# Kernel optimization log

Hardware: AMD Instinct MI355X
Metric: run time of the kernel (lower is better)

## Reference

```python
import jax, jax.numpy as jnp
import numpy as np

B, N, F = 128, 4096, 32
E, H, DEPTH, OUT = 16, 7, 3, 2
EH = E * H


def _ln(x, g, b, eps=1e-6):
    m = jnp.mean(x, axis=-1, keepdims=True)
    v = jnp.mean(jnp.square(x - m), axis=-1, keepdims=True)
    return (x - m) / jnp.sqrt(v + eps) * g + b


def setup_inputs() -> dict:
    key = jax.random.key(0)
    ks = jax.random.split(key, 24)
    s = 0.05
    inp = {
        "X": jax.random.normal(ks[0], (B, N, F), jnp.float32),
        "avail": jax.random.randint(ks[1], (B, N), 0, 2, jnp.int32),
        "W_enc1": jax.random.normal(ks[2], (F, E), jnp.float32) * s,
        "b_enc1": jnp.zeros((E,), jnp.float32),
        "W_enc2": jax.random.normal(ks[3], (E, E), jnp.float32) * s,
        "b_enc2": jnp.zeros((E,), jnp.float32),
        "W_enc3": jax.random.normal(ks[4], (E, E), jnp.float32) * s,
        "b_enc3": jnp.zeros((E,), jnp.float32),
        "g_enc": jnp.ones((E,), jnp.float32),
        "be_enc": jnp.zeros((E,), jnp.float32),
        "W_agg": jax.random.normal(ks[5], (DEPTH, E, H), jnp.float32) * s,
        "b_agg": jnp.zeros((DEPTH, H), jnp.float32),
        "W_phi1": jax.random.normal(ks[6], (DEPTH, E, EH), jnp.float32) * s,
        "b_phi1": jnp.zeros((DEPTH, EH), jnp.float32),
        "W_phi2": jax.random.normal(ks[7], (DEPTH, EH, EH), jnp.float32) * s,
        "b_phi2": jnp.zeros((DEPTH, EH), jnp.float32),
        "g_phi": jnp.ones((DEPTH, EH), jnp.float32),
        "be_phi": jnp.zeros((DEPTH, EH), jnp.float32),
        "W_proj": jax.random.normal(ks[8], (E, OUT), jnp.float32) * s,
        "b_proj": jnp.zeros((OUT,), jnp.float32),
    }
    return inp


def reference(X, avail, W_enc1, b_enc1, W_enc2, b_enc2, W_enc3, b_enc3, g_enc, be_enc,
              W_agg, b_agg, W_phi1, b_phi1, W_phi2, b_phi2, g_phi, be_phi, W_proj, b_proj):
    # init encoder: Dense-relu, Dense-relu, Dense, LayerNorm  -> Z: [B, N, E]
    Z = jax.nn.relu(X @ W_enc1 + b_enc1)
    Z = jax.nn.relu(Z @ W_enc2 + b_enc2)
    Z = Z @ W_enc3 + b_enc3
    Z = _ln(Z, g_enc, be_enc)
    X_embd = Z

    af = avail.astype(Z.dtype)                      # [B, N]
    num_avail = jnp.maximum(jnp.sum(af, axis=1), 1.0)  # [B]

    for d in range(DEPTH):
        # block_type='qua': fc(Z^2) -> [B, N, H]
        fcZ = jnp.square(Z) @ W_agg[d] + b_agg[d]
        # masked mean over the set axis -> Zbar: [B, H]
        Zbar = jnp.einsum('bnh,bn->bh', fcZ, af) / num_avail[:, None]
        # NonlinearMap(X_embd): Dense-relu-Dense-LayerNorm -> [B, N, E*H]
        phi = jax.nn.relu(X_embd @ W_phi1[d] + b_phi1[d])
        phi = phi @ W_phi2[d] + b_phi2[d]
        phi = _ln(phi, g_phi[d], be_phi[d])
        phi_rs = phi.reshape(phi.shape[0], phi.shape[1], H, E)  # [B, N, H, E]
        # delta = mean_h(phi_rs * Zbar[:,None,:,None]) -> [B, N, E]
        delta = jnp.einsum('bnhe,bh->bne', phi_rs, Zbar) / H
        Z = Z + delta

    return Z @ W_proj + b_proj  # [B, N, OUT]
```

## Files before the change

### kernel.cpp

```cpp
#include <hip/hip_runtime.h>
#include <hip/hip_bf16.h>

#define Bb 128
#define Nn 4096
#define Ff 32
#define Ee 16
#define Hh 7
#define EH 112
#define NROW (Bb*Nn)
#define PS 136
#define TPB_TILES 16
#define NBLK (NROW/16/TPB_TILES)

typedef __attribute__((ext_vector_type(8))) short  bf16x8;
typedef __attribute__((ext_vector_type(4))) float  f32x4;
typedef __attribute__((ext_vector_type(4))) unsigned int u32x4;
typedef __attribute__((ext_vector_type(2))) unsigned int u32x2;

__device__ inline unsigned pack2(float a, float b) {
    __hip_bfloat162 h = __float22bfloat162_rn(make_float2(a, b));
    return *reinterpret_cast<unsigned*>(&h);
}
union BF8 { unsigned u[4]; bf16x8 v; u32x4 q; };

__global__ __launch_bounds__(256) void enc_kernel(
    const float* __restrict__ X,
    const float* __restrict__ W1, const float* __restrict__ b1,
    const float* __restrict__ W2, const float* __restrict__ b2,
    const float* __restrict__ W3, const float* __restrict__ b3,
    const float* __restrict__ g,  const float* __restrict__ be,
    unsigned short* __restrict__ XeBF, float* __restrict__ Z)
{
    __shared__ float sW1[Ff*Ee], sW2[Ee*Ee], sW3[Ee*Ee];
    __shared__ float sb1[Ee], sb2[Ee], sb3[Ee], sg[Ee], sbe[Ee];
    int tid = threadIdx.x;
    for (int i = tid; i < Ff*Ee; i += 256) sW1[i] = W1[i];
    for (int i = tid; i < Ee*Ee; i += 256) { sW2[i] = W2[i]; sW3[i] = W3[i]; }
    if (tid < Ee) { sb1[tid]=b1[tid]; sb2[tid]=b2[tid]; sb3[tid]=b3[tid];
                    sg[tid]=g[tid];   sbe[tid]=be[tid]; }
    __syncthreads();

    size_t row = (size_t)blockIdx.x * 256u + (unsigned)tid;
    const float4* xr = reinterpret_cast<const float4*>(X + row * Ff);
    float x[Ff];
    #pragma unroll
    for (int i = 0; i < Ff/4; ++i) {
        float4 v = xr[i];
        x[4*i+0]=v.x; x[4*i+1]=v.y; x[4*i+2]=v.z; x[4*i+3]=v.w;
    }
    float h1[Ee];
    #pragma unroll
    for (int e = 0; e < Ee; ++e) h1[e] = sb1[e];
    #pragma unroll 4
    for (int k = 0; k < Ff; ++k) {
        float xk = x[k];
        #pragma unroll
        for (int e = 0; e < Ee; ++e) h1[e] = fmaf(xk, sW1[k*Ee+e], h1[e]);
    }
    #pragma unroll
    for (int e = 0; e < Ee; ++e) h1[e] = fmaxf(h1[e], 0.f);

    float h2[Ee];
    #pragma unroll
    for (int e = 0; e < Ee; ++e) h2[e] = sb2[e];
    #pragma unroll 4
    for (int k = 0; k < Ee; ++k) {
        float hk = h1[k];
        #pragma unroll
        for (int e = 0; e < Ee; ++e) h2[e] = fmaf(hk, sW2[k*Ee+e], h2[e]);
    }
    #pragma unroll
    for (int e = 0; e < Ee; ++e) h2[e] = fmaxf(h2[e], 0.f);

    float z[Ee];
    #pragma unroll
    for (int e = 0; e < Ee; ++e) z[e] = sb3[e];
    #pragma unroll 4
    for (int k = 0; k < Ee; ++k) {
        float hk = h2[k];
        #pragma unroll
        for (int e = 0; e < Ee; ++e) z[e] = fmaf(hk, sW3[k*Ee+e], z[e]);
    }
    float m = 0.f;
    #pragma unroll
    for (int e = 0; e < Ee; ++e) m += z[e];
    m *= (1.f/Ee);
    float v = 0.f;
    #pragma unroll
    for (int e = 0; e < Ee; ++e) { float d = z[e]-m; v += d*d; }
    v *= (1.f/Ee);
    float inv = rsqrtf(v + 1e-6f);
    #pragma unroll
    for (int e = 0; e < Ee; ++e) z[e] = (z[e]-m)*inv*sg[e] + sbe[e];

    float4* zo = reinterpret_cast<float4*>(Z + row*Ee);
    #pragma unroll
    for (int i = 0; i < Ee/4; ++i) {
        float4 o; o.x=z[4*i]; o.y=z[4*i+1]; o.z=z[4*i+2]; o.w=z[4*i+3];
        zo[i] = o;
    }
    unsigned us[8];
    #pragma unroll
    for (int j = 0; j < 8; ++j) us[j] = pack2(z[2*j], z[2*j+1]);
    u32x4 lo = {us[0],us[1],us[2],us[3]};
    u32x4 hi = {us[4],us[5],us[6],us[7]};
    u32x4* xo = reinterpret_cast<u32x4*>(XeBF + row*Ee);
    xo[0] = lo; xo[1] = hi;
}

__global__ __launch_bounds__(256) void wpack(
    const float* __restrict__ W_phi2, const float* __restrict__ W_phi1,
    unsigned short* __restrict__ W2F, unsigned short* __restrict__ W1F)
{
    int idx = blockIdx.x*256 + threadIdx.x;
    if (idx < 3*28*64) {
        int d = idx / (28*64); int r = idx % (28*64);
        int f = r >> 6, l = r & 63;
        int lg = l >> 4, li = l & 15, mt = f >> 2, kt = f & 3;
        const float* W2g = W_phi2 + (size_t)d*EH*EH;
        unsigned v[4];
        #pragma unroll
        for (int jj = 0; jj < 4; ++jj) {
            int k0 = kt*32 + lg*8 + jj*2;
            float a = (k0   < EH) ? W2g[(size_t)k0*EH     + mt*16 + li] : 0.f;
            float c = (k0+1 < EH) ? W2g[(size_t)(k0+1)*EH + mt*16 + li] : 0.f;
            v[jj] = pack2(a, c);
        }
        u32x4 q = {v[0], v[1], v[2], v[3]};
        *reinterpret_cast<u32x4*>(W2F + (size_t)idx*8) = q;
    } else if (idx < 3*28*64 + 3*7*64) {
        int r2 = idx - 3*28*64;
        int d = r2 / (7*64); int r = r2 % (7*64);
        int mt = r >> 6, l = r & 63;
        int g = l >> 4, i = l & 15;
        const float* W1g = W_phi1 + (size_t)d*Ee*EH;
        unsigned v[4];
        #pragma unroll
        for (int jj = 0; jj < 4; ++jj) {
            float a = 0.f, c = 0.f;
            if (g < 2) {
                a = W1g[(size_t)(g*8 + jj*2)  *EH + mt*16 + i];
                c = W1g[(size_t)(g*8 + jj*2+1)*EH + mt*16 + i];
            }
            v[jj] = pack2(a, c);
        }
        u32x4 q = {v[0], v[1], v[2], v[3]};
        *reinterpret_cast<u32x4*>(W1F + (size_t)r2*8) = q;
    }
}

__global__ __launch_bounds__(256) void zbar_part(
    const float* __restrict__ Z, const int* __restrict__ avail,
    const float* __restrict__ Wagg, const float* __restrict__ bagg,
    float* __restrict__ part)
{
    __shared__ float sW[Ee*Hh];
    __shared__ float sb[Hh];
    __shared__ float red[256][8];
    int b = blockIdx.x >> 3, p = blockIdx.x & 7;
    int tid = threadIdx.x;
    if (tid < Ee*Hh) sW[tid] = Wagg[tid];
    if (tid < Hh)    sb[tid] = bagg[tid];
    __syncthreads();

    float acc[Hh]; float cnt = 0.f;
    #pragma unroll
    for (int h = 0; h < Hh; ++h) acc[h] = 0.f;

    #pragma unroll
    for (int it = 0; it < 2; ++it) {
        int n = p*512 + it*256 + tid;
        size_t row = (size_t)b*Nn + n;
        const float4* zr = reinterpret_cast<const float4*>(Z + row*Ee);
        float zs[Ee];
        #pragma unroll
        for (int i = 0; i < Ee/4; ++i) {
            float4 v = zr[i];
            zs[4*i+0]=v.x*v.x; zs[4*i+1]=v.y*v.y; zs[4*i+2]=v.z*v.z; zs[4*i+3]=v.w*v.w;
        }
        float fc[Hh];
        #pragma unroll
        for (int h = 0; h < Hh; ++h) fc[h] = sb[h];
        #pragma unroll 4
        for (int e = 0; e < Ee; ++e) {
            float ze = zs[e];
            #pragma unroll
            for (int h = 0; h < Hh; ++h) fc[h] = fmaf(ze, sW[e*Hh+h], fc[h]);
        }
        float af = (float)avail[(size_t)b*Nn + n];
        #pragma unroll
        for (int h = 0; h < Hh; ++h) acc[h] = fmaf(af, fc[h], acc[h]);
        cnt += af;
    }
    #pragma unroll
    for (int h = 0; h < Hh; ++h) red[tid][h] = acc[h];
    red[tid][7] = cnt;
    __syncthreads();
    for (int s = 128; s > 0; s >>= 1) {
        if (tid < s) {
            #pragma unroll
            for (int i = 0; i < 8; ++i) red[tid][i] += red[tid+s][i];
        }
        __syncthreads();
    }
    if (tid < 8) part[((size_t)b*8 + p)*8 + tid] = red[0][tid];
}

__global__ __launch_bounds__(1024) void zbar_fin(
    const float* __restrict__ part, float* __restrict__ Zbar)
{
    int tid = threadIdx.x;
    int b = tid >> 3, h = tid & 7;
    float s = 0.f;
    #pragma unroll
    for (int p = 0; p < 8; ++p) s += part[((size_t)b*8 + p)*8 + h];
    float cnt = __shfl(s, (tid & 63) | 7);
    if (h < Hh) Zbar[b*Hh + h] = s / fmaxf(cnt, 1.f);
}

template<bool LAST>
__global__ __launch_bounds__(256, 3) void phi_mfma(
    const unsigned short* __restrict__ Xe,
    float* __restrict__ Z,
    const float* __restrict__ Zbar,
    const unsigned short* __restrict__ W1F,
    const unsigned short* __restrict__ W2F,
    const float* __restrict__ b1g, const float* __restrict__ b2g,
    const float* __restrict__ gg,  const float* __restrict__ beg,
    const float* __restrict__ Wp,  const float* __restrict__ bp,
    float* __restrict__ out)
{
    __shared__ __align__(16) unsigned short sW2F[28*512];
    __shared__ __align__(16) unsigned short sP1[4][16*PS];
    __shared__ __align__(16) float sB1[EH], sB2[EH];

    int tid  = threadIdx.x;
    int wave = tid >> 6, lane = tid & 63;
    int g = lane >> 4, i = lane & 15;

    for (int p = tid; p < 28*64; p += 256)
        *reinterpret_cast<u32x4*>(&sW2F[p*8]) =
            *reinterpret_cast<const u32x4*>(W2F + (size_t)p*8);
    for (int p = tid; p < (4*16*PS)/8; p += 256) {
        u32x4 zq = {0u,0u,0u,0u};
        reinterpret_cast<u32x4*>(&sP1[0][0])[p] = zq;
    }
    if (tid < EH) { sB1[tid] = b1g[tid]; sB2[tid] = b2g[tid]; }

    bf16x8 aW1[7];
    #pragma unroll
    for (int mt = 0; mt < 7; ++mt)
        aW1[mt] = *reinterpret_cast<const bf16x8*>(W1F + (size_t)(mt*64 + lane)*8);

    int b = blockIdx.x / (Nn/(TPB_TILES*16));
    f32x4 gz[7];
    float Gz[4] = {0,0,0,0}, Bz[4] = {0,0,0,0};
    #pragma unroll
    for (int mt = 0; mt < 7; ++mt) {
        float zbm = Zbar[b*Hh + mt] * (1.f/Hh);
        f32x4 pg = *reinterpret_cast<const f32x4*>(gg  + mt*16 + 4*g);
        f32x4 pe = *reinterpret_cast<const f32x4*>(beg + mt*16 + 4*g);
        #pragma unroll
        for (int r = 0; r < 4; ++r) {
            float gzv = pg[r] * zbm;
            gz[mt][r] = gzv;
            Gz[r] += gzv;
            Bz[r] += pe[r] * zbm;
        }
    }
    float wpa[4] = {0,0,0,0}, wpb[4] = {0,0,0,0}, bp0 = 0.f, bp1 = 0.f;
    if (LAST) {
        f32x4 u0 = *reinterpret_cast<const f32x4*>(Wp + 8*g);
        f32x4 u1 = *reinterpret_cast<const f32x4*>(Wp + 8*g + 4);
        wpa[0]=u0[0]; wpa[1]=u0[2]; wpa[2]=u1[0]; wpa[3]=u1[2];
        wpb[0]=u0[1]; wpb[1]=u0[3]; wpb[2]=u1[1]; wpb[3]=u1[3];
        bp0 = bp[0]; bp1 = bp[1];
    }
    __syncthreads();

    unsigned short* myP1 = &sP1[wave][0];
    size_t r0 = (size_t)(blockIdx.x*TPB_TILES + wave*4) * 16;

    BF8 zzu; zzu.u[0]=zzu.u[1]=zzu.u[2]=zzu.u[3]=0u;
    bf16x8 bx0 = zzu.v, bx1 = zzu.v, bx2 = zzu.v, bx3 = zzu.v;
    if (g < 2) {
        const unsigned short* xp = Xe + (r0 + i)*Ee + g*8;
        bx0 = *reinterpret_cast<const bf16x8*>(xp);
        bx1 = *reinterpret_cast<const bf16x8*>(xp + 16*Ee);
        bx2 = *reinterpret_cast<const bf16x8*>(xp + 32*Ee);
        bx3 = *reinterpret_cast<const bf16x8*>(xp + 48*Ee);
    }
    const float* zp = Z + (r0 + i)*Ee + 4*g;
    f32x4 zv0 = *reinterpret_cast<const f32x4*>(zp);
    f32x4 zv1 = *reinterpret_cast<const f32x4*>(zp + 16*Ee);
    f32x4 zv2 = *reinterpret_cast<const f32x4*>(zp + 32*Ee);
    f32x4 zv3 = *reinterpret_cast<const f32x4*>(zp + 48*Ee);

    auto tileop = [&](bf16x8 bx, f32x4 zv, size_t row0) {
        #pragma unroll
        for (int mt = 0; mt < 7; ++mt) {
            f32x4 c = *reinterpret_cast<const f32x4*>(&sB1[mt*16 + 4*g]);
            f32x4 d = __builtin_amdgcn_mfma_f32_16x16x32_bf16(aW1[mt], bx, c, 0, 0, 0);
            #pragma unroll
            for (int r = 0; r < 4; ++r) d[r] = fmaxf(d[r], 0.f);
            u32x2 w = {pack2(d[0], d[1]), pack2(d[2], d[3])};
            *reinterpret_cast<u32x2*>(&myP1[i*PS + mt*16 + 4*g]) = w;
        }
        f32x4 d2[7];
        #pragma unroll
        for (int mt = 0; mt < 7; ++mt)
            d2[mt] = *reinterpret_cast<const f32x4*>(&sB2[mt*16 + 4*g]);
        #pragma unroll
        for (int kt = 0; kt < 4; ++kt) {
            bf16x8 bpv = *reinterpret_cast<const bf16x8*>(&myP1[i*PS + kt*32 + 8*g]);
            #pragma unroll
            for (int mt = 0; mt < 7; ++mt) {
                bf16x8 a = *reinterpret_cast<const bf16x8*>(&sW2F[(mt*4 + kt)*512 + lane*8]);
                d2[mt] = __builtin_amdgcn_mfma_f32_16x16x32_bf16(a, bpv, d2[mt], 0, 0, 0);
            }
        }
        float s = 0.f;
        #pragma unroll
        for (int mt = 0; mt < 7; ++mt) s += d2[mt][0] + d2[mt][1] + d2[mt][2] + d2[mt][3];
        s += __shfl_xor(s, 16); s += __shfl_xor(s, 32);
        float m = s * (1.f/EH);
        float q = 0.f;
        #pragma unroll
        for (int mt = 0; mt < 7; ++mt) {
            #pragma unroll
            for (int r = 0; r < 4; ++r) { float dd = d2[mt][r] - m; q = fmaf(dd, dd, q); }
        }
        q += __shfl_xor(q, 16); q += __shfl_xor(q, 32);
        float inv = rsqrtf(q*(1.f/EH) + 1e-6f);

        float S1[4] = {0,0,0,0};
        #pragma unroll
        for (int mt = 0; mt < 7; ++mt) {
            #pragma unroll
            for (int r = 0; r < 4; ++r) S1[r] = fmaf(d2[mt][r], gz[mt][r], S1[r]);
        }
        f32x4 zn;
        #pragma unroll
        for (int r = 0; r < 4; ++r)
            zn[r] = zv[r] + (fmaf(-m, Gz[r], S1[r]) * inv + Bz[r]);

        if (!LAST) {
            *reinterpret_cast<f32x4*>(Z + (row0 + i)*Ee + 4*g) = zn;
        } else {
            float o0 = zn[0]*wpa[0] + zn[1]*wpa[1] + zn[2]*wpa[2] + zn[3]*wpa[3];
            float o1 = zn[0]*wpb[0] + zn[1]*wpb[1] + zn[2]*wpb[2] + zn[3]*wpb[3];
            o0 += __shfl_xor(o0, 16); o0 += __shfl_xor(o0, 32);
            o1 += __shfl_xor(o1, 16); o1 += __shfl_xor(o1, 32);
            if (g == 0) {
                float2 o; o.x = o0 + bp0; o.y = o1 + bp1;
                *reinterpret_cast<float2*>(out + (row0 + i)*2) = o;
            }
        }
    };

    tileop(bx0, zv0, r0);
    tileop(bx1, zv1, r0 + 16);
    tileop(bx2, zv2, r0 + 32);
    tileop(bx3, zv3, r0 + 48);
}

extern "C" void kernel_launch(void* const* d_in, const int* in_sizes, int n_in,
                              void* d_out, int out_size, void* d_ws, size_t ws_size,
                              hipStream_t stream)
{
    const float* X      = (const float*)d_in[0];
    const int*   avail  = (const int*)  d_in[1];
    const float* W_enc1 = (const float*)d_in[2];  const float* b_enc1 = (const float*)d_in[3];
    const float* W_enc2 = (const float*)d_in[4];  const float* b_enc2 = (const float*)d_in[5];
    const float* W_enc3 = (const float*)d_in[6];  const float* b_enc3 = (const float*)d_in[7];
    const float* g_enc  = (const float*)d_in[8];  const float* be_enc = (const float*)d_in[9];
    const float* W_agg  = (const float*)d_in[10]; const float* b_agg  = (const float*)d_in[11];
    const float* W_phi1 = (const float*)d_in[12]; const float* b_phi1 = (const float*)d_in[13];
    const float* W_phi2 = (const float*)d_in[14]; const float* b_phi2 = (const float*)d_in[15];
    const float* g_phi  = (const float*)d_in[16]; const float* be_phi = (const float*)d_in[17];
    const float* W_proj = (const float*)d_in[18]; const float* b_proj = (const float*)d_in[19];
    float* out = (float*)d_out;

    char* ws = (char*)d_ws;
    unsigned short* XeBF = (unsigned short*)ws;
    float* Z   = (float*)(ws + (size_t)NROW*Ee*2);
    char*  p   = ws + (size_t)NROW*Ee*2 + (size_t)NROW*Ee*4;
    float* Zb  = (float*)p;                 p += 4096;
    float* part= (float*)p;                 p += (size_t)Bb*8*8*4;
    unsigned short* W2F = (unsigned short*)p; p += (size_t)3*28*512*2;
    unsigned short* W1F = (unsigned short*)p;

    wpack<<<(3*28*64 + 3*7*64 + 255)/256, 256, 0, stream>>>(W_phi2, W_phi1, W2F, W1F);

    enc_kernel<<<NROW/256, 256, 0, stream>>>(
        X, W_enc1, b_enc1, W_enc2, b_enc2, W_enc3, b_enc3, g_enc, be_enc, XeBF, Z);

    for (int d = 0; d < 3; ++d) {
        zbar_part<<<Bb*8, 256, 0, stream>>>(
            Z, avail, W_agg + d*Ee*Hh, b_agg + d*Hh, part);
        zbar_fin<<<1, 1024, 0, stream>>>(part, Zb);
        if (d < 2) {
            phi_mfma<false><<<NBLK, 256, 0, stream>>>(
                XeBF, Z, Zb,
                W1F + (size_t)d*7*512, W2F + (size_t)d*28*512,
                b_phi1 + d*EH, b_phi2 + d*EH,
                g_phi + d*EH, be_phi + d*EH, W_proj, b_proj, out);
        } else {
            phi_mfma<true><<<NBLK, 256, 0, stream>>>(
                XeBF, Z, Zb,
                W1F + (size_t)d*7*512, W2F + (size_t)d*28*512,
                b_phi1 + d*EH, b_phi2 + d*EH,
                g_phi + d*EH, be_phi + d*EH, W_proj, b_proj, out);
        }
    }
}
```

Baseline: 209.1 us.

## Fuse masked-mean reductions into encoder and phi kernels, store Z as bf16

Removes the separate zbar_part/zbar_fin kernels. The encoder and each non-final phi kernel now compute the next depth's masked squared aggregation and accumulate per-batch sums with atomics, and the bias terms are folded into the packed weight matrices through a constant-one column. Z is now kept in bf16 rather than fp32, which cuts global traffic, and MFMA tiles are processed in pairs using double-buffered LDS. The aims are fewer launches, fewer re-reads of Z and better MFMA overlap, at the cost of precision, atomic non-determinism and lower occupancy (launch bounds 2 instead of 3).

After: 167.9 us. 1.25x faster.

```diff
diff --git a/kernel.cpp b/kernel.cpp
--- a/kernel.cpp
+++ b/kernel.cpp
@@ -9,8 +9,7 @@
 #define EH 112
 #define NROW (Bb*Nn)
 #define PS 136
-#define TPB_TILES 16
-#define NBLK (NROW/16/TPB_TILES)
+#define NBLK 2048
 
 typedef __attribute__((ext_vector_type(8))) short  bf16x8;
 typedef __attribute__((ext_vector_type(4))) float  f32x4;
@@ -29,15 +28,19 @@
     const float* __restrict__ W2, const float* __restrict__ b2,
     const float* __restrict__ W3, const float* __restrict__ b3,
     const float* __restrict__ g,  const float* __restrict__ be,
-    unsigned short* __restrict__ XeBF, float* __restrict__ Z)
+    const float* __restrict__ Wagg0, const int* __restrict__ avail,
+    unsigned short* __restrict__ XeBF, float* __restrict__ acc0)
 {
     __shared__ float sW1[Ff*Ee], sW2[Ee*Ee], sW3[Ee*Ee];
     __shared__ float sb1[Ee], sb2[Ee], sb3[Ee], sg[Ee], sbe[Ee];
+    __shared__ float sWq[Ee*Hh];
+    __shared__ float red[256][8];
     int tid = threadIdx.x;
     for (int i = tid; i < Ff*Ee; i += 256) sW1[i] = W1[i];
     for (int i = tid; i < Ee*Ee; i += 256) { sW2[i] = W2[i]; sW3[i] = W3[i]; }
     if (tid < Ee) { sb1[tid]=b1[tid]; sb2[tid]=b2[tid]; sb3[tid]=b3[tid];
                     sg[tid]=g[tid];   sbe[tid]=be[tid]; }
+    if (tid < Ee*Hh) sWq[tid] = Wagg0[tid];
     __syncthreads();
 
     size_t row = (size_t)blockIdx.x * 256u + (unsigned)tid;
@@ -93,12 +96,6 @@
     #pragma unroll
     for (int e = 0; e < Ee; ++e) z[e] = (z[e]-m)*inv*sg[e] + sbe[e];
 
-    float4* zo = reinterpret_cast<float4*>(Z + row*Ee);
-    #pragma unroll
-    for (int i = 0; i < Ee/4; ++i) {
-        float4 o; o.x=z[4*i]; o.y=z[4*i+1]; o.z=z[4*i+2]; o.w=z[4*i+3];
-        zo[i] = o;
-    }
     unsigned us[8];
     #pragma unroll
     for (int j = 0; j < 8; ++j) us[j] = pack2(z[2*j], z[2*j+1]);
@@ -106,10 +103,34 @@
     u32x4 hi = {us[4],us[5],us[6],us[7]};
     u32x4* xo = reinterpret_cast<u32x4*>(XeBF + row*Ee);
     xo[0] = lo; xo[1] = hi;
+
+    float af = (float)avail[row];
+    float fc[Hh];
+    #pragma unroll
+    for (int h = 0; h < Hh; ++h) fc[h] = 0.f;
+    #pragma unroll
+    for (int e = 0; e < Ee; ++e) {
+        float z2 = z[e]*z[e];
+        #pragma unroll
+        for (int h = 0; h < Hh; ++h) fc[h] = fmaf(z2, sWq[e*Hh+h], fc[h]);
+    }
+    #pragma unroll
+    for (int h = 0; h < Hh; ++h) red[tid][h] = af * fc[h];
+    red[tid][7] = af;
+    __syncthreads();
+    for (int s = 128; s > 0; s >>= 1) {
+        if (tid < s) {
+            #pragma unroll
+            for (int q2 = 0; q2 < 8; ++q2) red[tid][q2] += red[tid+s][q2];
+        }
+        __syncthreads();
+    }
+    if (tid < 8) atomicAdd(&acc0[(blockIdx.x >> 4)*8 + tid], red[0][tid]);
 }
 
 __global__ __launch_bounds__(256) void wpack(
     const float* __restrict__ W_phi2, const float* __restrict__ W_phi1,
+    const float* __restrict__ b_phi1, const float* __restrict__ b_phi2,
     unsigned short* __restrict__ W2F, unsigned short* __restrict__ W1F)
 {
     int idx = blockIdx.x*256 + threadIdx.x;
@@ -118,12 +139,15 @@
         int f = r >> 6, l = r & 63;
         int lg = l >> 4, li = l & 15, mt = f >> 2, kt = f & 3;
         const float* W2g = W_phi2 + (size_t)d*EH*EH;
+        const float* b2g = b_phi2 + (size_t)d*EH;
+        int mm = mt*16 + li;
         unsigned v[4];
         #pragma unroll
         for (int jj = 0; jj < 4; ++jj) {
             int k0 = kt*32 + lg*8 + jj*2;
-            float a = (k0   < EH) ? W2g[(size_t)k0*EH     + mt*16 + li] : 0.f;
-            float c = (k0+1 < EH) ? W2g[(size_t)(k0+1)*EH + mt*16 + li] : 0.f;
+            float a = (k0 < EH) ? W2g[(size_t)k0*EH + mm]
+                                : (k0 == EH ? b2g[mm] : 0.f);
+            float c = (k0+1 < EH) ? W2g[(size_t)(k0+1)*EH + mm] : 0.f;
             v[jj] = pack2(a, c);
         }
         u32x4 q = {v[0], v[1], v[2], v[3]};
@@ -134,13 +158,17 @@
         int mt = r >> 6, l = r & 63;
         int g = l >> 4, i = l & 15;
         const float* W1g = W_phi1 + (size_t)d*Ee*EH;
+        const float* b1g = b_phi1 + (size_t)d*EH;
+        int mm = mt*16 + i;
         unsigned v[4];
         #pragma unroll
         for (int jj = 0; jj < 4; ++jj) {
             float a = 0.f, c = 0.f;
             if (g < 2) {
-                a = W1g[(size_t)(g*8 + jj*2)  *EH + mt*16 + i];
-                c = W1g[(size_t)(g*8 + jj*2+1)*EH + mt*16 + i];
+                a = W1g[(size_t)(g*8 + jj*2)  *EH + mm];
+                c = W1g[(size_t)(g*8 + jj*2+1)*EH + mm];
+            } else if (g == 2 && jj == 0) {
+                a = b1g[mm];
             }
             v[jj] = pack2(a, c);
         }
@@ -149,90 +177,23 @@
     }
 }
 
-__global__ __launch_bounds__(256) void zbar_part(
-    const float* __restrict__ Z, const int* __restrict__ avail,
-    const float* __restrict__ Wagg, const float* __restrict__ bagg,
-    float* __restrict__ part)
-{
-    __shared__ float sW[Ee*Hh];
-    __shared__ float sb[Hh];
-    __shared__ float red[256][8];
-    int b = blockIdx.x >> 3, p = blockIdx.x & 7;
-    int tid = threadIdx.x;
-    if (tid < Ee*Hh) sW[tid] = Wagg[tid];
-    if (tid < Hh)    sb[tid] = bagg[tid];
-    __syncthreads();
-
-    float acc[Hh]; float cnt = 0.f;
-    #pragma unroll
-    for (int h = 0; h < Hh; ++h) acc[h] = 0.f;
-
-    #pragma unroll
-    for (int it = 0; it < 2; ++it) {
-        int n = p*512 + it*256 + tid;
-        size_t row = (size_t)b*Nn + n;
-        const float4* zr = reinterpret_cast<const float4*>(Z + row*Ee);
-        float zs[Ee];
-        #pragma unroll
-        for (int i = 0; i < Ee/4; ++i) {
-            float4 v = zr[i];
-            zs[4*i+0]=v.x*v.x; zs[4*i+1]=v.y*v.y; zs[4*i+2]=v.z*v.z; zs[4*i+3]=v.w*v.w;
-        }
-        float fc[Hh];
-        #pragma unroll
-        for (int h = 0; h < Hh; ++h) fc[h] = sb[h];
-        #pragma unroll 4
-        for (int e = 0; e < Ee; ++e) {
-            float ze = zs[e];
-            #pragma unroll
-            for (int h = 0; h < Hh; ++h) fc[h] = fmaf(ze, sW[e*Hh+h], fc[h]);
-        }
-        float af = (float)avail[(size_t)b*Nn + n];
-        #pragma unroll
-        for (int h = 0; h < Hh; ++h) acc[h] = fmaf(af, fc[h], acc[h]);
-        cnt += af;
-    }
-    #pragma unroll
-    for (int h = 0; h < Hh; ++h) red[tid][h] = acc[h];
-    red[tid][7] = cnt;
-    __syncthreads();
-    for (int s = 128; s > 0; s >>= 1) {
-        if (tid < s) {
-            #pragma unroll
-            for (int i = 0; i < 8; ++i) red[tid][i] += red[tid+s][i];
-        }
-        __syncthreads();
-    }
-    if (tid < 8) part[((size_t)b*8 + p)*8 + tid] = red[0][tid];
-}
-
-__global__ __launch_bounds__(1024) void zbar_fin(
-    const float* __restrict__ part, float* __restrict__ Zbar)
-{
-    int tid = threadIdx.x;
-    int b = tid >> 3, h = tid & 7;
-    float s = 0.f;
-    #pragma unroll
-    for (int p = 0; p < 8; ++p) s += part[((size_t)b*8 + p)*8 + h];
-    float cnt = __shfl(s, (tid & 63) | 7);
-    if (h < Hh) Zbar[b*Hh + h] = s / fmaxf(cnt, 1.f);
-}
-
 template<bool LAST>
-__global__ __launch_bounds__(256, 3) void phi_mfma(
+__global__ __launch_bounds__(256, 2) void phi_mfma(
+    const unsigned short* __restrict__ Zin,
     const unsigned short* __restrict__ Xe,
-    float* __restrict__ Z,
-    const float* __restrict__ Zbar,
+    unsigned short* __restrict__ Zout,
+    const float* __restrict__ accIn, const float* __restrict__ baggD,
+    const float* __restrict__ WaggN, float* __restrict__ accN,
+    const int* __restrict__ avail,
     const unsigned short* __restrict__ W1F,
     const unsigned short* __restrict__ W2F,
-    const float* __restrict__ b1g, const float* __restrict__ b2g,
     const float* __restrict__ gg,  const float* __restrict__ beg,
     const float* __restrict__ Wp,  const float* __restrict__ bp,
     float* __restrict__ out)
 {
     __shared__ __align__(16) unsigned short sW2F[28*512];
-    __shared__ __align__(16) unsigned short sP1[4][16*PS];
-    __shared__ __align__(16) float sB1[EH], sB2[EH];
+    __shared__ __align__(16) unsigned short sP1[4][2][16*PS];
+    __shared__ float sRed[4][8];
 
     int tid  = threadIdx.x;
     int wave = tid >> 6, lane = tid & 63;
@@ -241,32 +202,50 @@
     for (int p = tid; p < 28*64; p += 256)
         *reinterpret_cast<u32x4*>(&sW2F[p*8]) =
             *reinterpret_cast<const u32x4*>(W2F + (size_t)p*8);
-    for (int p = tid; p < (4*16*PS)/8; p += 256) {
+    for (int p = tid; p < (4*2*16*PS)/8; p += 256) {
         u32x4 zq = {0u,0u,0u,0u};
-        reinterpret_cast<u32x4*>(&sP1[0][0])[p] = zq;
-    }
-    if (tid < EH) { sB1[tid] = b1g[tid]; sB2[tid] = b2g[tid]; }
-
+        reinterpret_cast<u32x4*>(&sP1[0][0][0])[p] = zq;
+    }
+    __syncthreads();
+    if (tid < 128) {
+        int w = tid >> 5, bb = (tid >> 4) & 1, r = tid & 15;
+        sP1[w][bb][r*PS + 112] = 0x3F80;
+    }
+
+    int b = blockIdx.x >> 4;
+    float cntb = accIn[b*8 + 7];
+    float cden = fmaxf(cntb, 1.f);
+    float zb[Hh];
+    #pragma unroll
+    for (int h = 0; h < Hh; ++h)
+        zb[h] = (accIn[b*8 + h] + baggD[h]*cntb) / cden * (1.f/Hh);
+
+    f32x4 gz[7];
+    float Gz[4] = {0,0,0,0}, Bz[4] = {0,0,0,0};
+    #pragma unroll
+    for (int mt = 0; mt < 7; ++mt) {
+        f32x4 pg = *reinterpret_cast<const f32x4*>(gg  + mt*16 + 4*g);
+        f32x4 pe = *reinterpret_cast<const f32x4*>(beg + mt*16 + 4*g);
+        #pragma unroll
+        for (int r = 0; r < 4; ++r) {
+            float gzv = pg[r] * zb[mt];
+            gz[mt][r] = gzv;
+            Gz[r] += gzv;
+            Bz[r] += pe[r] * zb[mt];
+        }
+    }
     bf16x8 aW1[7];
     #pragma unroll
     for (int mt = 0; mt < 7; ++mt)
         aW1[mt] = *reinterpret_cast<const bf16x8*>(W1F + (size_t)(mt*64 + lane)*8);
 
-    int b = blockIdx.x / (Nn/(TPB_TILES*16));
-    f32x4 gz[7];
-    float Gz[4] = {0,0,0,0}, Bz[4] = {0,0,0,0};
-    #pragma unroll
-    for (int mt = 0; mt < 7; ++mt) {
-        float zbm = Zbar[b*Hh + mt] * (1.f/Hh);
-        f32x4 pg = *reinterpret_cast<const f32x4*>(gg  + mt*16 + 4*g);
-        f32x4 pe = *reinterpret_cast<const f32x4*>(beg + mt*16 + 4*g);
-        #pragma unroll
-        for (int r = 0; r < 4; ++r) {
-            float gzv = pg[r] * zbm;
-            gz[mt][r] = gzv;
-            Gz[r] += gzv;
-            Bz[r] += pe[r] * zbm;
-        }
+    f32x4 wq[7];
+    if (!LAST) {
+        #pragma unroll
+        for (int h = 0; h < Hh; ++h)
+            #pragma unroll
+            for (int r = 0; r < 4; ++r)
+                wq[h][r] = WaggN[(4*g + r)*Hh + h];
     }
     float wpa[4] = {0,0,0,0}, wpb[4] = {0,0,0,0}, bp0 = 0.f, bp1 = 0.f;
     if (LAST) {
@@ -276,13 +255,15 @@
         wpb[0]=u0[1]; wpb[1]=u0[3]; wpb[2]=u1[1]; wpb[3]=u1[3];
         bp0 = bp[0]; bp1 = bp[1];
     }
+    float wacc[Hh] = {0,0,0,0,0,0,0};
+    float wcnt = 0.f;
     __syncthreads();
 
-    unsigned short* myP1 = &sP1[wave][0];
-    size_t r0 = (size_t)(blockIdx.x*TPB_TILES + wave*4) * 16;
-
-    BF8 zzu; zzu.u[0]=zzu.u[1]=zzu.u[2]=zzu.u[3]=0u;
-    bf16x8 bx0 = zzu.v, bx1 = zzu.v, bx2 = zzu.v, bx3 = zzu.v;
+    size_t r0 = (size_t)(blockIdx.x*16 + wave*4) * 16;
+
+    BF8 bz_; bz_.u[0]=bz_.u[1]=bz_.u[2]=bz_.u[3]=0u;
+    if (g == 2) bz_.u[0] = 0x00003F80u;
+    bf16x8 bx0 = bz_.v, bx1 = bz_.v, bx2 = bz_.v, bx3 = bz_.v;
     if (g < 2) {
         const unsigned short* xp = Xe + (r0 + i)*Ee + g*8;
         bx0 = *reinterpret_cast<const bf16x8*>(xp);
@@ -290,45 +271,27 @@
         bx2 = *reinterpret_cast<const bf16x8*>(xp + 32*Ee);
         bx3 = *reinterpret_cast<const bf16x8*>(xp + 48*Ee);
     }
-    const float* zp = Z + (r0 + i)*Ee + 4*g;
-    f32x4 zv0 = *reinterpret_cast<const f32x4*>(zp);
-    f32x4 zv1 = *reinterpret_cast<const f32x4*>(zp + 16*Ee);
-    f32x4 zv2 = *reinterpret_cast<const f32x4*>(zp + 32*Ee);
-    f32x4 zv3 = *reinterpret_cast<const f32x4*>(zp + 48*Ee);
-
-    auto tileop = [&](bf16x8 bx, f32x4 zv, size_t row0) {
-        #pragma unroll
-        for (int mt = 0; mt < 7; ++mt) {
-            f32x4 c = *reinterpret_cast<const f32x4*>(&sB1[mt*16 + 4*g]);
-            f32x4 d = __builtin_amdgcn_mfma_f32_16x16x32_bf16(aW1[mt], bx, c, 0, 0, 0);
-            #pragma unroll
-            for (int r = 0; r < 4; ++r) d[r] = fmaxf(d[r], 0.f);
-            u32x2 w = {pack2(d[0], d[1]), pack2(d[2], d[3])};
-            *reinterpret_cast<u32x2*>(&myP1[i*PS + mt*16 + 4*g]) = w;
-        }
-        f32x4 d2[7];
-        #pragma unroll
-        for (int mt = 0; mt < 7; ++mt)
-            d2[mt] = *reinterpret_cast<const f32x4*>(&sB2[mt*16 + 4*g]);
-        #pragma unroll
-        for (int kt = 0; kt < 4; ++kt) {
-            bf16x8 bpv = *reinterpret_cast<const bf16x8*>(&myP1[i*PS + kt*32 + 8*g]);
-            #pragma unroll
-            for (int mt = 0; mt < 7; ++mt) {
-                bf16x8 a = *reinterpret_cast<const bf16x8*>(&sW2F[(mt*4 + kt)*512 + lane*8]);
-                d2[mt] = __builtin_amdgcn_mfma_f32_16x16x32_bf16(a, bpv, d2[mt], 0, 0, 0);
-            }
-        }
+    const unsigned short* zp = Zin + (r0 + i)*Ee + 4*g;
+    u32x2 zu0 = *reinterpret_cast<const u32x2*>(zp);
+    u32x2 zu1 = *reinterpret_cast<const u32x2*>(zp + 16*Ee);
+    u32x2 zu2 = *reinterpret_cast<const u32x2*>(zp + 32*Ee);
+    u32x2 zu3 = *reinterpret_cast<const u32x2*>(zp + 48*Ee);
+
+    unsigned short* p1A = &sP1[wave][0][0];
+    unsigned short* p1B = &sP1[wave][1][0];
+    const f32x4 zz = {0.f,0.f,0.f,0.f};
+
+    auto epi = [&](const f32x4* d2, u32x2 zu, size_t row0) {
         float s = 0.f;
         #pragma unroll
-        for (int mt = 0; mt < 7; ++mt) s += d2[mt][0] + d2[mt][1] + d2[mt][2] + d2[mt][3];
+        for (int mt = 0; mt < 7; ++mt) s += d2[mt][0]+d2[mt][1]+d2[mt][2]+d2[mt][3];
         s += __shfl_xor(s, 16); s += __shfl_xor(s, 32);
         float m = s * (1.f/EH);
         float q = 0.f;
         #pragma unroll
         for (int mt = 0; mt < 7; ++mt) {
             #pragma unroll
-            for (int r = 0; r < 4; ++r) { float dd = d2[mt][r] - m; q = fmaf(dd, dd, q); }
+            for (int r = 0; r < 4; ++r) { float dd = d2[mt][r]-m; q = fmaf(dd,dd,q); }
         }
         q += __shfl_xor(q, 16); q += __shfl_xor(q, 32);
         float inv = rsqrtf(q*(1.f/EH) + 1e-6f);
@@ -339,13 +302,30 @@
             #pragma unroll
             for (int r = 0; r < 4; ++r) S1[r] = fmaf(d2[mt][r], gz[mt][r], S1[r]);
         }
-        f32x4 zn;
+        unsigned lo = zu[0], hi = zu[1];
+        float zv[4];
+        zv[0] = __uint_as_float((lo & 0xFFFFu) << 16);
+        zv[1] = __uint_as_float(lo & 0xFFFF0000u);
+        zv[2] = __uint_as_float((hi & 0xFFFFu) << 16);
+        zv[3] = __uint_as_float(hi & 0xFFFF0000u);
+        float zn[4];
         #pragma unroll
         for (int r = 0; r < 4; ++r)
             zn[r] = zv[r] + (fmaf(-m, Gz[r], S1[r]) * inv + Bz[r]);
 
         if (!LAST) {
-            *reinterpret_cast<f32x4*>(Z + (row0 + i)*Ee + 4*g) = zn;
+            u32x2 w = {pack2(zn[0], zn[1]), pack2(zn[2], zn[3])};
+            *reinterpret_cast<u32x2*>(Zout + (row0 + i)*Ee + 4*g) = w;
+            float af = (float)avail[row0 + i];
+            float z20 = zn[0]*zn[0], z21 = zn[1]*zn[1];
+            float z22 = zn[2]*zn[2], z23 = zn[3]*zn[3];
+            #pragma unroll
+            for (int h = 0; h < Hh; ++h) {
+                float f = z20*wq[h][0] + z21*wq[h][1] + z22*wq[h][2] + z23*wq[h][3];
+                f += __shfl_xor(f, 16); f += __shfl_xor(f, 32);
+                wacc[h] = fmaf(af, f, wacc[h]);
+            }
+            wcnt += af;
         } else {
             float o0 = zn[0]*wpa[0] + zn[1]*wpa[1] + zn[2]*wpa[2] + zn[3]*wpa[3];
             float o1 = zn[0]*wpb[0] + zn[1]*wpb[1] + zn[2]*wpb[2] + zn[3]*wpb[3];
@@ -358,10 +338,56 @@
         }
     };
 
-    tileop(bx0, zv0, r0);
-    tileop(bx1, zv1, r0 + 16);
-    tileop(bx2, zv2, r0 + 32);
-    tileop(bx3, zv3, r0 + 48);
+    auto pair = [&](bf16x8 bxA, bf16x8 bxB, u32x2 zuA, u32x2 zuB, size_t rowA) {
+        #pragma unroll
+        for (int mt = 0; mt < 7; ++mt) {
+            f32x4 dA = __builtin_amdgcn_mfma_f32_16x16x32_bf16(aW1[mt], bxA, zz, 0,0,0);
+            f32x4 dB = __builtin_amdgcn_mfma_f32_16x16x32_bf16(aW1[mt], bxB, zz, 0,0,0);
+            #pragma unroll
+            for (int r = 0; r < 4; ++r) { dA[r] = fmaxf(dA[r],0.f); dB[r] = fmaxf(dB[r],0.f); }
+            u32x2 wA = {pack2(dA[0],dA[1]), pack2(dA[2],dA[3])};
+            u32x2 wB = {pack2(dB[0],dB[1]), pack2(dB[2],dB[3])};
+            *reinterpret_cast<u32x2*>(&p1A[i*PS + mt*16 + 4*g]) = wA;
+            *reinterpret_cast<u32x2*>(&p1B[i*PS + mt*16 + 4*g]) = wB;
+        }
+        f32x4 d2A[7], d2B[7];
+        #pragma unroll
+        for (int mt = 0; mt < 7; ++mt) { d2A[mt] = zz; d2B[mt] = zz; }
+        #pragma unroll
+        for (int kt = 0; kt < 4; ++kt) {
+            bf16x8 bpA = *reinterpret_cast<const bf16x8*>(&p1A[i*PS + kt*32 + 8*g]);
+            bf16x8 bpB = *reinterpret_cast<const bf16x8*>(&p1B[i*PS + kt*32 + 8*g]);
+            #pragma unroll
+            for (int mt = 0; mt < 7; ++mt) {
+                bf16x8 a = *reinterpret_cast<const bf16x8*>(&sW2F[(mt*4 + kt)*512 + lane*8]);
+                d2A[mt] = __builtin_amdgcn_mfma_f32_16x16x32_bf16(a, bpA, d2A[mt], 0,0,0);
+                d2B[mt] = __builtin_amdgcn_mfma_f32_16x16x32_bf16(a, bpB, d2B[mt], 0,0,0);
+            }
+        }
+        epi(d2A, zuA, rowA);
+        epi(d2B, zuB, rowA + 16);
+    };
+
+    pair(bx0, bx1, zu0, zu1, r0);
+    pair(bx2, bx3, zu2, zu3, r0 + 32);
+
+    if (!LAST) {
+        #pragma unroll
+        for (int off = 1; off < 64; off <<= 1) {
+            #pragma unroll
+            for (int h = 0; h < Hh; ++h) wacc[h] += __shfl_xor(wacc[h], off);
+            wcnt += __shfl_xor(wcnt, off);
+        }
+        if (lane == 0) {
+            #pragma unroll
+            for (int h = 0; h < Hh; ++h) sRed[wave][h] = wacc[h]*0.25f;
+            sRed[wave][7] = wcnt*0.25f;
+        }
+        __syncthreads();
+        if (tid < 8)
+            atomicAdd(&accN[b*8 + tid],
+                      sRed[0][tid]+sRed[1][tid]+sRed[2][tid]+sRed[3][tid]);
+    }
 }
 
 extern "C" void kernel_launch(void* const* d_in, const int* in_sizes, int n_in,
@@ -383,34 +409,31 @@
 
     char* ws = (char*)d_ws;
     unsigned short* XeBF = (unsigned short*)ws;
-    float* Z   = (float*)(ws + (size_t)NROW*Ee*2);
-    char*  p   = ws + (size_t)NROW*Ee*2 + (size_t)NROW*Ee*4;
-    float* Zb  = (float*)p;                 p += 4096;
-    float* part= (float*)p;                 p += (size_t)Bb*8*8*4;
+    unsigned short* Zb   = (unsigned short*)(ws + (size_t)NROW*Ee*2);
+    char* p = ws + 2*(size_t)NROW*Ee*2;
+    float* acc = (float*)p;                  p += 3*Bb*8*sizeof(float);
     unsigned short* W2F = (unsigned short*)p; p += (size_t)3*28*512*2;
     unsigned short* W1F = (unsigned short*)p;
 
-    wpack<<<(3*28*64 + 3*7*64 + 255)/256, 256, 0, stream>>>(W_phi2, W_phi1, W2F, W1F);
-
-    enc_kernel<<<NROW/256, 256, 0, stream>>>(
-        X, W_enc1, b_enc1, W_enc2, b_enc2, W_enc3, b_enc3, g_enc, be_enc, XeBF, Z);
-
-    for (int d = 0; d < 3; ++d) {
-        zbar_part<<<Bb*8, 256, 0, stream>>>(
-            Z, avail, W_agg + d*Ee*Hh, b_agg + d*Hh, part);
-        zbar_fin<<<1, 1024, 0, stream>>>(part, Zb);
-        if (d < 2) {
-            phi_mfma<false><<<NBLK, 256, 0, stream>>>(
-                XeBF, Z, Zb,
-                W1F + (size_t)d*7*512, W2F + (size_t)d*28*512,
-                b_phi1 + d*EH, b_phi2 + d*EH,
-                g_phi + d*EH, be_phi + d*EH, W_proj, b_proj, out);
-        } else {
-            phi_mfma<true><<<NBLK, 256, 0, stream>>>(
-                XeBF, Z, Zb,
-                W1F + (size_t)d*7*512, W2F + (size_t)d*28*512,
-                b_phi1 + d*EH, b_phi2 + d*EH,
-                g_phi + d*EH, be_phi + d*EH, W_proj, b_proj, out);
-        }
-    }
+    hipMemsetAsync(acc, 0, 3*Bb*8*sizeof(float), stream);
+    wpack<<<(3*28*64 + 3*7*64 + 255)/256, 256, 0, stream>>>(
+        W_phi2, W_phi1, b_phi1, b_phi2, W2F, W1F);
+
+    enc_kernel<<<NBLK, 256, 0, stream>>>(
+        X, W_enc1, b_enc1, W_enc2, b_enc2, W_enc3, b_enc3, g_enc, be_enc,
+        W_agg, avail, XeBF, acc);
+
+    phi_mfma<false><<<NBLK, 256, 0, stream>>>(
+        XeBF, XeBF, Zb, acc, b_agg, W_agg + Ee*Hh, acc + Bb*8, avail,
+        W1F, W2F, g_phi, be_phi, W_proj, b_proj, out);
+
+    phi_mfma<false><<<NBLK, 256, 0, stream>>>(
+        Zb, XeBF, Zb, acc + Bb*8, b_agg + Hh, W_agg + 2*Ee*Hh, acc + 2*Bb*8, avail,
+        W1F + (size_t)7*512, W2F + (size_t)28*512,
+        g_phi + EH, be_phi + EH, W_proj, b_proj, out);
+
+    phi_mfma<true><<<NBLK, 256, 0, stream>>>(
+        Zb, XeBF, Zb, acc + 2*Bb*8, b_agg + 2*Hh, W_agg, acc, avail,
+        W1F + (size_t)14*512, W2F + (size_t)56*512,
+        g_phi + 2*EH, be_phi + 2*EH, W_proj, b_proj, out);
 }
```
